# Performance work log

Hardware: AMD Instinct MI355X
Metric: run time of the kernel (lower is better)

The kernel has to match this reference:

```python
import jax, jax.numpy as jnp
import numpy as np

DIM = 768
HID = 3072
HID2 = HID // 2
MAX_LEVEL = 8
N_LEV = MAX_LEVEL + 1
BATCH, SEQ = 2, 2048
EPS = 1e-5


def _layernorm(x, gamma, beta):
    m = jnp.mean(x, axis=-1, keepdims=True)
    v = jnp.mean(jnp.square(x - m), axis=-1, keepdims=True)
    return (x - m) * jax.lax.rsqrt(v + EPS) * gamma + beta


def setup_inputs() -> dict:
    key = jax.random.key(0)
    ks = jax.random.split(key, 12)
    s = 0.02
    return {
        "x": jax.random.normal(ks[0], (BATCH, SEQ, DIM), dtype=jnp.float32),
        "levels_info": jax.random.randint(ks[1], (SEQ, 4), 0, N_LEV, dtype=jnp.int32),
        "gamma": jnp.ones((DIM,), dtype=jnp.float32),
        "beta": jnp.zeros((DIM,), dtype=jnp.float32),
        "W1": jax.random.normal(ks[2], (DIM, HID), dtype=jnp.float32) * s,
        "b1": jnp.zeros((HID,), dtype=jnp.float32),
        "W2": jax.random.normal(ks[3], (HID, DIM), dtype=jnp.float32) * s,
        "b2": jnp.zeros((DIM,), dtype=jnp.float32),
        "A1": jax.random.normal(ks[4], (N_LEV, DIM, HID2), dtype=jnp.float32) * s,
        "a1b": jnp.zeros((N_LEV, HID2), dtype=jnp.float32),
        "A2": jax.random.normal(ks[5], (N_LEV, HID2, DIM), dtype=jnp.float32) * s,
        "a2b": jnp.zeros((N_LEV, DIM), dtype=jnp.float32),
        "lmw": jnp.ones((N_LEV,), dtype=jnp.float32)
        + jax.random.normal(ks[6], (N_LEV,), dtype=jnp.float32) * 0.1,
    }


def reference(x, levels_info, gamma, beta, W1, b1, W2, b2, A1, a1b, A2, a2b, lmw):
    # x: [B,S,D]
    x_norm = _layernorm(x, gamma, beta)
    # main MLP: Linear -> GELU (exact, torch default) -> Linear; dropout=0 is identity
    h = jax.nn.gelu(jnp.einsum("bsd,dh->bsh", x_norm, W1) + b1, approximate=False)
    main_out = jnp.einsum("bsh,hd->bsd", h, W2) + b2

    # per-token depth-indexed adapter routing
    depths = jnp.clip(levels_info[:, 0], 0, MAX_LEVEL)  # [S]
    level_adapted = jnp.zeros_like(main_out)
    for lvl in range(N_LEV):  # small fixed expert set
        mask = (depths == lvl).astype(x.dtype)[None, :, None]  # [1,S,1]
        hl = jax.nn.relu(jnp.einsum("bsd,dh->bsh", x_norm, A1[lvl]) + a1b[lvl])
        level_adapted = level_adapted + mask * (
            jnp.einsum("bsh,hd->bsd", hl, A2[lvl]) + a2b[lvl]
        )

    # softmax over the sequence axis (faithful to F.softmax(..., dim=0))
    mix = jax.nn.softmax(lmw[depths], axis=0)[None, :, None]  # [1,S,1]
    return main_out * (1.0 - mix) + level_adapted * mix
```

## Files before the change

### kernel.cpp

```cpp
#include <hip/hip_runtime.h>
#include <hip/hip_bf16.h>
#include <math.h>

typedef __bf16 bf16;
typedef __bf16 bf16x4 __attribute__((ext_vector_type(4)));
typedef __bf16 bf16x8 __attribute__((ext_vector_type(8)));
typedef float f32x4 __attribute__((ext_vector_type(4)));

#define DIM 768
#define HID 3072
#define HID2 1536
#define NLEV 9
#define SEQ 2048
#define ROWS 4096
#define MAXPAD 5248
#define MAXTILES 41

__device__ __forceinline__ void gld16(const void* g, void* l) {
    __builtin_amdgcn_global_load_lds(
        (const __attribute__((address_space(1))) void*)g,
        (__attribute__((address_space(3))) void*)l, 16, 0, 0);
}

__device__ __forceinline__ float fast_gelu(float v) {
    float v2 = v * v;
    float twou = v * (1.59576912f + 0.071354816f * v2);
    float t = __expf(twou);
    return v * t / (t + 1.0f);
}


__device__ __forceinline__ void ln4_body(int blk,
                                         const float* __restrict__ x,
                                         const float* __restrict__ gamma,
                                         const float* __restrict__ beta,
                                         bf16* __restrict__ xn) {
    int tid = threadIdx.x;
    int wv = tid >> 6, ln = tid & 63;
    int row = blk * 4 + wv;
    const float* xr = x + (size_t)row * DIM;
    int c = ln * 4;
    float4 v0 = *(const float4*)(xr + c);
    float4 v1 = *(const float4*)(xr + c + 256);
    float4 v2 = *(const float4*)(xr + c + 512);
    float s = v0.x + v0.y + v0.z + v0.w
            + v1.x + v1.y + v1.z + v1.w
            + v2.x + v2.y + v2.z + v2.w;
    float q = v0.x * v0.x + v0.y * v0.y + v0.z * v0.z + v0.w * v0.w
            + v1.x * v1.x + v1.y * v1.y + v1.z * v1.z + v1.w * v1.w
            + v2.x * v2.x + v2.y * v2.y + v2.z * v2.z + v2.w * v2.w;
#pragma unroll
    for (int off = 32; off; off >>= 1) {
        s += __shfl_xor(s, off, 64);
        q += __shfl_xor(q, off, 64);
    }
    float m = s * (1.0f / DIM);
    float r = rsqrtf(q * (1.0f / DIM) - m * m + 1e-5f);
    bf16* xo = xn + (size_t)row * DIM;
#pragma unroll
    for (int p = 0; p < 3; p++) {
        int cc = c + p * 256;
        float4 v = (p == 0) ? v0 : (p == 1) ? v1 : v2;
        float4 g = *(const float4*)(gamma + cc);
        float4 b = *(const float4*)(beta + cc);
        bf16x4 o;
        o[0] = (bf16)((v.x - m) * r * g.x + b.x);
        o[1] = (bf16)((v.y - m) * r * g.y + b.y);
        o[2] = (bf16)((v.z - m) * r * g.z + b.z);
        o[3] = (bf16)((v.w - m) * r * g.w + b.w);
        *(bf16x4*)(xo + cc) = o;
    }
}

__device__ __forceinline__ void transpose_body64(bf16* sm,
                                                 const float* __restrict__ inb,
                                                 bf16* __restrict__ outb,
                                                 int R, int C, int bx, int by) {
    int tid = threadIdx.x;
    int ty = tid >> 4;
    int tx4 = (tid & 15) * 4;
#pragma unroll
    for (int p = 0; p < 4; p++) {
        int rloc = p * 16 + ty;
        int row = by * 64 + rloc;
        float4 v = *(const float4*)(inb + (size_t)row * C + bx * 64 + tx4);
        bf16x4 o;
        o[0] = (bf16)v.x; o[1] = (bf16)v.y; o[2] = (bf16)v.z; o[3] = (bf16)v.w;
        *(bf16x4*)(sm + rloc * 68 + tx4) = o;
    }
    __syncthreads();
    int ch = tid & 7;
    int ocb = tid >> 3;
#pragma unroll
    for (int p = 0; p < 2; p++) {
        int oc = p * 32 + ocb;
        bf16x8 tmp;
#pragma unroll
        for (int k = 0; k < 8; k++) tmp[k] = sm[(ch * 8 + k) * 68 + oc];
        *(bf16x8*)(outb + (size_t)(bx * 64 + oc) * R + by * 64 + ch * 8) = tmp;
    }
}

__device__ __forceinline__ void routing_body(float* sm,
                                             const int* __restrict__ levels_info,
                                             const float* __restrict__ lmw,
                                             float* __restrict__ mix,
                                             int* __restrict__ row_index,
                                             int* __restrict__ tile_meta,
                                             float* __restrict__ zbuf) {
    int* cnt = (int*)sm;
    int* cur = cnt + NLEV;
    int* off = cur + NLEV;
    float* mixv = (float*)(off + NLEV);
    int tid = threadIdx.x;
    if (tid < NLEV) { cnt[tid] = 0; cur[tid] = 0; }
    __syncthreads();
    for (int s = tid; s < SEQ; s += 256) {
        int d = levels_info[s * 4];
        d = d < 0 ? 0 : (d > 8 ? 8 : d);
        atomicAdd(&cnt[d], 1);
    }
    for (int i = tid; i < MAXPAD; i += 256) row_index[i] = -1;
    for (int i = tid; i < 512; i += 256) zbuf[i] = 0.0f;
    __syncthreads();
    if (tid == 0) {
        float mx = lmw[0];
        for (int l = 1; l < NLEV; l++) mx = fmaxf(mx, lmw[l]);
        float denom = 0.f;
        for (int l = 0; l < NLEV; l++) denom += (float)cnt[l] * expf(lmw[l] - mx);
        float inv = 1.0f / denom;
        int running = 0, t = 0;
        for (int l = 0; l < NLEV; l++) {
            mixv[l] = expf(lmw[l] - mx) * inv;
            off[l] = running;
            int seg = (2 * cnt[l] + 127) & ~127;
            for (int k = 0; k < seg / 128; k++) tile_meta[t++] = l;
            running += seg;
        }
        for (; t < MAXTILES; t++) tile_meta[t] = -1;
    }
    __syncthreads();
    for (int s = tid; s < SEQ; s += 256) {
        int d = levels_info[s * 4];
        d = d < 0 ? 0 : (d > 8 ? 8 : d);
        int p = atomicAdd(&cur[d], 2);
        row_index[off[d] + p]     = s;
        row_index[off[d] + p + 1] = s + SEQ;
        mix[s] = mixv[d];
    }
}

__global__ __launch_bounds__(256) void prep_kernel(const float* __restrict__ x,
                                                   const int* __restrict__ levels_info,
                                                   const float* __restrict__ gamma,
                                                   const float* __restrict__ beta,
                                                   const float* __restrict__ W1,
                                                   const float* __restrict__ A1,
                                                   const float* __restrict__ W2,
                                                   const float* __restrict__ A2,
                                                   const float* __restrict__ lmw,
                                                   bf16* __restrict__ Xn,
                                                   bf16* __restrict__ W1t,
                                                   bf16* __restrict__ A1t,
                                                   bf16* __restrict__ W2t,
                                                   bf16* __restrict__ A2t,
                                                   float* __restrict__ mix,
                                                   int* __restrict__ row_index,
                                                   int* __restrict__ tile_meta,
                                                   float* __restrict__ zbuf) {
    __shared__ __align__(16) bf16 tsm[64 * 68];
    int b = blockIdx.x;
    if (b == 0) { routing_body((float*)tsm, levels_info, lmw, mix, row_index, tile_meta, zbuf); return; }
    b -= 1;
    if (b < 1024) { ln4_body(b, x, gamma, beta, Xn); return; }
    b -= 1024;
    if (b < 576) {
        transpose_body64(tsm, W1, W1t, DIM, HID, b % 48, b / 48);
        return;
    }
    b -= 576;
    if (b < 2592) {
        int bz = b / 288, r = b % 288;
        transpose_body64(tsm, A1 + (size_t)bz * DIM * HID2, A1t + (size_t)bz * DIM * HID2,
                         DIM, HID2, r % 24, r / 24);
        return;
    }
    b -= 2592;
    if (b < 576) {
        transpose_body64(tsm, W2, W2t, HID, DIM, b % 12, b / 12);
        return;
    }
    b -= 576;
    {
        int bz = b / 288, r = b % 288;
        transpose_body64(tsm, A2 + (size_t)bz * HID2 * DIM, A2t + (size_t)bz * HID2 * DIM,
                         HID2, DIM, r % 12, r / 12);
    }
}

template<int KT>
__device__ __forceinline__ void gemm_loop_db(const bf16* ga0, const bf16* ga1,
                                             const bf16* gb0, const bf16* gb1,
                                             bf16* As, bf16* Bs,
                                             f32x4 (&acc)[4][4]) {
    int tid = threadIdx.x;
    int wv = tid >> 6;
    int lane = tid & 63;
    int wm = wv >> 1, wn = wv & 1;
    int swz = (lane >> 1) & 3;
    int achunk = ((lane >> 4) ^ swz) * 8;
    int aoff = ((wm * 64) + (lane & 15)) * 32 + achunk;
    int boff = ((wn * 64) + (lane & 15)) * 32 + achunk;
    gld16(ga0, As + wv * 512);
    gld16(ga1, As + 2048 + wv * 512);
    gld16(gb0, Bs + wv * 512);
    gld16(gb1, Bs + 2048 + wv * 512);
    ga0 += 32; ga1 += 32; gb0 += 32; gb1 += 32;
#pragma unroll
    for (int kt = 0; kt < KT; ++kt) {
        __syncthreads();
        const int cur = (kt & 1) << 12;
        const int nxt = cur ^ 4096;
        if (kt + 1 < KT) {
            gld16(ga0, As + nxt + wv * 512);
            gld16(ga1, As + nxt + 2048 + wv * 512);
            gld16(gb0, Bs + nxt + wv * 512);
            gld16(gb1, Bs + nxt + 2048 + wv * 512);
            ga0 += 32; ga1 += 32; gb0 += 32; gb1 += 32;
        }
        bf16x8 af[4], bfr[4];
#pragma unroll
        for (int i = 0; i < 4; i++) af[i] = *(const bf16x8*)(As + cur + aoff + i * 512);
#pragma unroll
        for (int j = 0; j < 4; j++) bfr[j] = *(const bf16x8*)(Bs + cur + boff + j * 512);
#pragma unroll
        for (int i = 0; i < 4; i++)
#pragma unroll
            for (int j = 0; j < 4; j++)
                acc[i][j] = __builtin_amdgcn_mfma_f32_16x16x32_bf16(af[i], bfr[j], acc[i][j], 0, 0, 0);
    }
}

#define ACC_INIT(acc) \
    _Pragma("unroll") for (int i = 0; i < 4; i++) \
    _Pragma("unroll") for (int j = 0; j < 4; j++) acc[i][j] = (f32x4){0.f, 0.f, 0.f, 0.f};

#define SWZ_CG(tid) (((tid) & 3) ^ (((tid) >> 3) & 3))

__device__ __forceinline__ void store_tile(const bf16* cbuf, int lane,
                                           bf16* gptr, int ldg) {
#pragma unroll
    for (int p = 0; p < 8; p++) {
        int lrow = p * 8 + (lane >> 3);
        int chunk = (lane & 7) * 8;
        bf16x8 v = *(const bf16x8*)(cbuf + lrow * 64 + chunk);
        *(bf16x8*)(gptr + (size_t)lrow * ldg + chunk) = v;
    }
}

__global__ __launch_bounds__(256) void mlp1_kernel(const bf16* __restrict__ Xn,
                                                   const bf16* __restrict__ W1t,
                                                   const float* __restrict__ b1,
                                                   bf16* __restrict__ H,
                                                   const bf16* __restrict__ A1t,
                                                   const float* __restrict__ a1b,
                                                   const int* __restrict__ row_index,
                                                   const int* __restrict__ tile_meta,
                                                   const bf16* __restrict__ zbuf,
                                                   bf16* __restrict__ HL) {
    __shared__ __align__(16) bf16 smem[16384];
    bf16* As = smem;
    bf16* Bs = smem + 8192;
    int bid = blockIdx.x, tid = threadIdx.x;
    int r0 = tid >> 2, cg = SWZ_CG(tid);
    int lane = tid & 63, wv = tid >> 6, wm = wv >> 1, wn = wv & 1;
    bf16* cbuf = smem + wv * 4096;

    if (bid < 768) {
        int nb = bid / 32, mb = bid % 32;
        f32x4 acc[4][4];
        ACC_INIT(acc);
        const bf16* ga0 = Xn + (size_t)(mb * 128 + r0) * DIM + cg * 8;
        const bf16* ga1 = ga0 + (size_t)64 * DIM;
        const bf16* gb0 = W1t + (size_t)(nb * 128 + r0) * DIM + cg * 8;
        const bf16* gb1 = gb0 + (size_t)64 * DIM;
        gemm_loop_db<24>(ga0, ga1, gb0, gb1, As, Bs, acc);
        int cbase = nb * 128 + wn * 64 + (lane & 15);
        __syncthreads();
#pragma unroll
        for (int j = 0; j < 4; j++) {
            float bias = b1[cbase + j * 16];
#pragma unroll
            for (int i = 0; i < 4; i++)
#pragma unroll
                for (int r = 0; r < 4; r++) {
                    int lrow = i * 16 + ((lane >> 4) << 2) + r;
                    int lcol = j * 16 + (lane & 15);
                    cbuf[lrow * 64 + lcol] = (bf16)fast_gelu(acc[i][j][r] + bias);
                }
        }
        __syncthreads();
        store_tile(cbuf, lane, H + (size_t)(mb * 128 + wm * 64) * HID + nb * 128 + wn * 64, HID);
    } else {
        int t2 = bid - 768;
        int nb = t2 % 12, t = t2 / 12;
        int lvl = tile_meta[t];
        if (lvl < 0) return;
        f32x4 acc[4][4];
        ACC_INIT(acc);
        int ridx0 = row_index[t * 128 + r0];
        int ridx1 = row_index[t * 128 + 64 + r0];
        const bf16* ga0 = (ridx0 >= 0) ? (Xn + (size_t)ridx0 * DIM + cg * 8) : (zbuf + cg * 8);
        const bf16* ga1 = (ridx1 >= 0) ? (Xn + (size_t)ridx1 * DIM + cg * 8) : (zbuf + cg * 8);
        const bf16* Bl = A1t + (size_t)lvl * HID2 * DIM;
        const bf16* gb0 = Bl + (size_t)(nb * 128 + r0) * DIM + cg * 8;
        const bf16* gb1 = gb0 + (size_t)64 * DIM;
        gemm_loop_db<24>(ga0, ga1, gb0, gb1, As, Bs, acc);
        int cbase = nb * 128 + wn * 64 + (lane & 15);
        __syncthreads();
#pragma unroll
        for (int j = 0; j < 4; j++) {
            float bias = a1b[lvl * HID2 + cbase + j * 16];
#pragma unroll
            for (int i = 0; i < 4; i++)
#pragma unroll
                for (int r = 0; r < 4; r++) {
                    int lrow = i * 16 + ((lane >> 4) << 2) + r;
                    int lcol = j * 16 + (lane & 15);
                    cbuf[lrow * 64 + lcol] = (bf16)fmaxf(acc[i][j][r] + bias, 0.0f);
                }
        }
        __syncthreads();
        store_tile(cbuf, lane, HL + (size_t)(t * 128 + wm * 64) * HID2 + nb * 128 + wn * 64, HID2);
    }
}

__global__ __launch_bounds__(256) void mlp2_kernel(const bf16* __restrict__ H,
                                                   const bf16* __restrict__ W2t,
                                                   bf16* __restrict__ part,
                                                   const bf16* __restrict__ HL,
                                                   const bf16* __restrict__ A2t,
                                                   const float* __restrict__ a2b,
                                                   const int* __restrict__ row_index,
                                                   const int* __restrict__ tile_meta,
                                                   bf16* __restrict__ apart) {
    __shared__ __align__(16) bf16 smem[16384];
    bf16* As = smem;
    bf16* Bs = smem + 8192;
    int bid = blockIdx.x, tid = threadIdx.x;
    int r0 = tid >> 2, cg = SWZ_CG(tid);
    int lane = tid & 63, wv = tid >> 6, wm = wv >> 1, wn = wv & 1;
    bf16* cbuf = smem + wv * 4096;
    f32x4 acc[4][4];
    ACC_INIT(acc);

    if (bid < 384) {
        int cc = bid % 12;
        int nb = cc >> 1, ks = cc & 1;
        int mb = bid / 12;
        const bf16* ga0 = H + (size_t)(mb * 128 + r0) * HID + ks * 1536 + cg * 8;
        const bf16* ga1 = ga0 + (size_t)64 * HID;
        const bf16* gb0 = W2t + (size_t)(nb * 128 + r0) * HID + ks * 1536 + cg * 8;
        const bf16* gb1 = gb0 + (size_t)64 * HID;
        gemm_loop_db<48>(ga0, ga1, gb0, gb1, As, Bs, acc);
        __syncthreads();
#pragma unroll
        for (int j = 0; j < 4; j++)
#pragma unroll
            for (int i = 0; i < 4; i++)
#pragma unroll
                for (int r = 0; r < 4; r++) {
                    int lrow = i * 16 + ((lane >> 4) << 2) + r;
                    int lcol = j * 16 + (lane & 15);
                    cbuf[lrow * 64 + lcol] = (bf16)acc[i][j][r];
                }
        __syncthreads();
        bf16* pk = part + (size_t)ks * ROWS * DIM;
        store_tile(cbuf, lane, pk + (size_t)(mb * 128 + wm * 64) * DIM + nb * 128 + wn * 64, DIM);
    } else {
        int t2 = bid - 384;
        int nb = t2 % 6, t = t2 / 6;
        int lvl = tile_meta[t];
        if (lvl < 0) return;
        const bf16* ga0 = HL + (size_t)(t * 128 + r0) * HID2 + cg * 8;
        const bf16* ga1 = ga0 + (size_t)64 * HID2;
        const bf16* Bl = A2t + (size_t)lvl * DIM * HID2;
        const bf16* gb0 = Bl + (size_t)(nb * 128 + r0) * HID2 + cg * 8;
        const bf16* gb1 = gb0 + (size_t)64 * HID2;
        gemm_loop_db<48>(ga0, ga1, gb0, gb1, As, Bs, acc);
        int cbase = nb * 128 + wn * 64 + (lane & 15);
        __syncthreads();
#pragma unroll
        for (int j = 0; j < 4; j++) {
            float bias = a2b[lvl * DIM + cbase + j * 16];
#pragma unroll
            for (int i = 0; i < 4; i++)
#pragma unroll
                for (int r = 0; r < 4; r++) {
                    int lrow = i * 16 + ((lane >> 4) << 2) + r;
                    int lcol = j * 16 + (lane & 15);
                    cbuf[lrow * 64 + lcol] = (bf16)(acc[i][j][r] + bias);
                }
        }
        __syncthreads();
        int colg = nb * 128 + wn * 64;
#pragma unroll
        for (int p = 0; p < 8; p++) {
            int lrow = p * 8 + (lane >> 3);
            int chunk = (lane & 7) * 8;
            int rg = row_index[t * 128 + wm * 64 + lrow];
            if (rg >= 0) {
                bf16x8 v = *(const bf16x8*)(cbuf + lrow * 64 + chunk);
                *(bf16x8*)(apart + (size_t)rg * DIM + colg + chunk) = v;
            }
        }
    }
}

__global__ __launch_bounds__(256) void combine_kernel(const bf16* __restrict__ part,
                                                      const bf16* __restrict__ apart,
                                                      const float* __restrict__ b2,
                                                      const float* __restrict__ mix,
                                                      float* __restrict__ out) {
    int i = blockIdx.x * 256 + threadIdx.x;
    int base = i * 4;
    int row = base / DIM;
    int c = base - row * DIM;
    float mx = mix[row & (SEQ - 1)];
    bf16x4 p0 = *(const bf16x4*)(part + base);
    bf16x4 p1 = *(const bf16x4*)(part + (size_t)ROWS * DIM + base);
    bf16x4 a0 = *(const bf16x4*)(apart + base);
    float4 o;
    float* po = &o.x;
#pragma unroll
    for (int k = 0; k < 4; k++) {
        float main_v = (float)p0[k] + (float)p1[k] + b2[c + k];
        po[k] = (1.0f - mx) * main_v + mx * (float)a0[k];
    }
    *(float4*)(out + base) = o;
}

extern "C" void kernel_launch(void* const* d_in, const int* in_sizes, int n_in,
                              void* d_out, int out_size, void* d_ws, size_t ws_size,
                              hipStream_t stream) {
    const float* x    = (const float*)d_in[0];
    const int* levels = (const int*)d_in[1];
    const float* gamma= (const float*)d_in[2];
    const float* beta = (const float*)d_in[3];
    const float* W1   = (const float*)d_in[4];
    const float* b1   = (const float*)d_in[5];
    const float* W2   = (const float*)d_in[6];
    const float* b2   = (const float*)d_in[7];
    const float* A1   = (const float*)d_in[8];
    const float* a1b  = (const float*)d_in[9];
    const float* A2   = (const float*)d_in[10];
    const float* a2b  = (const float*)d_in[11];
    const float* lmw  = (const float*)d_in[12];
    float* out = (float*)d_out;

    char* p = (char*)d_ws;
    auto alloc = [&](size_t bytes) {
        char* r = p;
        p += (bytes + 255) & ~(size_t)255;
        return r;
    };
    bf16* Xn   = (bf16*)alloc((size_t)ROWS * DIM * 2);
    bf16* W1t  = (bf16*)alloc((size_t)HID * DIM * 2);
    bf16* W2t  = (bf16*)alloc((size_t)DIM * HID * 2);
    bf16* A1t  = (bf16*)alloc((size_t)NLEV * HID2 * DIM * 2);
    bf16* A2t  = (bf16*)alloc((size_t)NLEV * DIM * HID2 * 2);
    bf16* H    = (bf16*)alloc((size_t)ROWS * HID * 2);
    bf16* HL   = (bf16*)alloc((size_t)MAXPAD * HID2 * 2);
    bf16* part = (bf16*)alloc((size_t)2 * ROWS * DIM * 2);
    bf16* apart= (bf16*)alloc((size_t)ROWS * DIM * 2);
    float* mix = (float*)alloc(SEQ * 4);
    int* row_index = (int*)alloc(MAXPAD * 4);
    int* tile_meta = (int*)alloc(MAXTILES * 4);
    float* zbuf    = (float*)alloc(2048);

    prep_kernel<<<dim3(1 + 1024 + 576 + 2592 + 576 + 2592), dim3(256), 0, stream>>>(
        x, levels, gamma, beta, W1, A1, W2, A2, lmw,
        Xn, W1t, A1t, W2t, A2t, mix, row_index, tile_meta, zbuf);

    mlp1_kernel<<<dim3(768 + 492), dim3(256), 0, stream>>>(
        Xn, W1t, b1, H, A1t, a1b, row_index, tile_meta, (const bf16*)zbuf, HL);

    mlp2_kernel<<<dim3(384 + MAXTILES * 6), dim3(256), 0, stream>>>(
        H, W2t, part, HL, A2t, a2b, row_index, tile_meta, apart);

    combine_kernel<<<dim3(ROWS * DIM / 1024), dim3(256), 0, stream>>>(
        part, apart, b2, mix, out);
}
```

Before: 280.6 us.

## Deepen GEMM K-tile to 64, add XCD block swizzle and grouped tile ordering

The double-buffered GEMM loop now stages 64-wide K slices instead of 32, which halves the number of barrier-separated iterations and doubles LDS use per block. The LDS layout changes to an XOR swizzle across 8 chunks. Block IDs are remapped with an XCD-aware swizzle, and the main MLP1 tiles are grouped so that neighbouring blocks share A/B panels in L2. The larger LDS footprint may lower occupancy, and the zero buffer is enlarged to cover 64-element reads for padded rows.

```diff
diff --git a/kernel.cpp b/kernel.cpp
--- a/kernel.cpp
+++ b/kernel.cpp
@@ -27,6 +27,12 @@
     float twou = v * (1.59576912f + 0.071354816f * v2);
     float t = __expf(twou);
     return v * t / (t + 1.0f);
+}
+
+__device__ __forceinline__ int xcd_swizzle(int s, int nwg) {
+    int q = nwg >> 3, r = nwg & 7;
+    int x = s & 7, i = s >> 3;
+    return (x < r ? x * (q + 1) : r * (q + 1) + (x - r) * q) + i;
 }
 
 
@@ -121,7 +127,7 @@
         atomicAdd(&cnt[d], 1);
     }
     for (int i = tid; i < MAXPAD; i += 256) row_index[i] = -1;
-    for (int i = tid; i < 512; i += 256) zbuf[i] = 0.0f;
+    for (int i = tid; i < 1024; i += 256) zbuf[i] = 0.0f;
     __syncthreads();
     if (tid == 0) {
         float mx = lmw[0];
@@ -199,53 +205,56 @@
 }
 
 template<int KT>
-__device__ __forceinline__ void gemm_loop_db(const bf16* ga0, const bf16* ga1,
-                                             const bf16* gb0, const bf16* gb1,
-                                             bf16* As, bf16* Bs,
-                                             f32x4 (&acc)[4][4]) {
+__device__ __forceinline__ void gemm_loop_db64(const bf16* (&ga)[4], const bf16* (&gb)[4],
+                                               bf16* As, bf16* Bs,
+                                               f32x4 (&acc)[4][4]) {
     int tid = threadIdx.x;
     int wv = tid >> 6;
     int lane = tid & 63;
     int wm = wv >> 1, wn = wv & 1;
-    int swz = (lane >> 1) & 3;
-    int achunk = ((lane >> 4) ^ swz) * 8;
-    int aoff = ((wm * 64) + (lane & 15)) * 32 + achunk;
-    int boff = ((wn * 64) + (lane & 15)) * 32 + achunk;
-    gld16(ga0, As + wv * 512);
-    gld16(ga1, As + 2048 + wv * 512);
-    gld16(gb0, Bs + wv * 512);
-    gld16(gb1, Bs + 2048 + wv * 512);
-    ga0 += 32; ga1 += 32; gb0 += 32; gb1 += 32;
+    int r = lane & 15;
+    int ch0 = ((lane >> 4) ^ (lane & 7)) * 8;
+    int aoff = (wm * 64 + r) * 64 + ch0;
+    int boff = (wn * 64 + r) * 64 + ch0;
+#pragma unroll
+    for (int c = 0; c < 4; c++) {
+        gld16(ga[c], As + (c * 32 + wv * 8) * 64);
+        gld16(gb[c], Bs + (c * 32 + wv * 8) * 64);
+        ga[c] += 64; gb[c] += 64;
+    }
 #pragma unroll
     for (int kt = 0; kt < KT; ++kt) {
         __syncthreads();
-        const int cur = (kt & 1) << 12;
-        const int nxt = cur ^ 4096;
+        const int cur = (kt & 1) << 13;
+        const int nxt = cur ^ 8192;
         if (kt + 1 < KT) {
-            gld16(ga0, As + nxt + wv * 512);
-            gld16(ga1, As + nxt + 2048 + wv * 512);
-            gld16(gb0, Bs + nxt + wv * 512);
-            gld16(gb1, Bs + nxt + 2048 + wv * 512);
-            ga0 += 32; ga1 += 32; gb0 += 32; gb1 += 32;
-        }
-        bf16x8 af[4], bfr[4];
-#pragma unroll
-        for (int i = 0; i < 4; i++) af[i] = *(const bf16x8*)(As + cur + aoff + i * 512);
-#pragma unroll
-        for (int j = 0; j < 4; j++) bfr[j] = *(const bf16x8*)(Bs + cur + boff + j * 512);
-#pragma unroll
-        for (int i = 0; i < 4; i++)
-#pragma unroll
-            for (int j = 0; j < 4; j++)
-                acc[i][j] = __builtin_amdgcn_mfma_f32_16x16x32_bf16(af[i], bfr[j], acc[i][j], 0, 0, 0);
+#pragma unroll
+            for (int c = 0; c < 4; c++) {
+                gld16(ga[c], As + nxt + (c * 32 + wv * 8) * 64);
+                gld16(gb[c], Bs + nxt + (c * 32 + wv * 8) * 64);
+                ga[c] += 64; gb[c] += 64;
+            }
+        }
+#pragma unroll
+        for (int k32 = 0; k32 < 2; k32++) {
+            const int kx = k32 << 5;
+            bf16x8 af[4], bfr[4];
+#pragma unroll
+            for (int i = 0; i < 4; i++) af[i] = *(const bf16x8*)(As + cur + ((aoff + i * 1024) ^ kx));
+#pragma unroll
+            for (int j = 0; j < 4; j++) bfr[j] = *(const bf16x8*)(Bs + cur + ((boff + j * 1024) ^ kx));
+#pragma unroll
+            for (int i = 0; i < 4; i++)
+#pragma unroll
+                for (int j = 0; j < 4; j++)
+                    acc[i][j] = __builtin_amdgcn_mfma_f32_16x16x32_bf16(af[i], bfr[j], acc[i][j], 0, 0, 0);
+        }
     }
 }
 
 #define ACC_INIT(acc) \
     _Pragma("unroll") for (int i = 0; i < 4; i++) \
     _Pragma("unroll") for (int j = 0; j < 4; j++) acc[i][j] = (f32x4){0.f, 0.f, 0.f, 0.f};
-
-#define SWZ_CG(tid) (((tid) & 3) ^ (((tid) >> 3) & 3))
 
 __device__ __forceinline__ void store_tile(const bf16* cbuf, int lane,
                                            bf16* gptr, int ldg) {
@@ -268,23 +277,30 @@
                                                    const int* __restrict__ tile_meta,
                                                    const bf16* __restrict__ zbuf,
                                                    bf16* __restrict__ HL) {
-    __shared__ __align__(16) bf16 smem[16384];
+    __shared__ __align__(16) bf16 smem[32768];
     bf16* As = smem;
-    bf16* Bs = smem + 8192;
-    int bid = blockIdx.x, tid = threadIdx.x;
-    int r0 = tid >> 2, cg = SWZ_CG(tid);
+    bf16* Bs = smem + 16384;
+    int bid = xcd_swizzle(blockIdx.x, 1260);
+    int tid = threadIdx.x;
     int lane = tid & 63, wv = tid >> 6, wm = wv >> 1, wn = wv & 1;
+    int lrow = lane >> 3;
+    int lch = ((lane & 7) ^ lrow) * 8;
     bf16* cbuf = smem + wv * 4096;
 
     if (bid < 768) {
-        int nb = bid / 32, mb = bid % 32;
+        int s = bid >> 5, u = bid & 31;
+        int nb = (s % 6) * 4 + (u & 3);
+        int mb = (s / 6) * 8 + (u >> 2);
         f32x4 acc[4][4];
         ACC_INIT(acc);
-        const bf16* ga0 = Xn + (size_t)(mb * 128 + r0) * DIM + cg * 8;
-        const bf16* ga1 = ga0 + (size_t)64 * DIM;
-        const bf16* gb0 = W1t + (size_t)(nb * 128 + r0) * DIM + cg * 8;
-        const bf16* gb1 = gb0 + (size_t)64 * DIM;
-        gemm_loop_db<24>(ga0, ga1, gb0, gb1, As, Bs, acc);
+        const bf16* ga[4]; const bf16* gb[4];
+#pragma unroll
+        for (int c = 0; c < 4; c++) {
+            int rt = c * 32 + wv * 8 + lrow;
+            ga[c] = Xn  + (size_t)(mb * 128 + rt) * DIM + lch;
+            gb[c] = W1t + (size_t)(nb * 128 + rt) * DIM + lch;
+        }
+        gemm_loop_db64<12>(ga, gb, As, Bs, acc);
         int cbase = nb * 128 + wn * 64 + (lane & 15);
         __syncthreads();
 #pragma unroll
@@ -294,9 +310,9 @@
             for (int i = 0; i < 4; i++)
 #pragma unroll
                 for (int r = 0; r < 4; r++) {
-                    int lrow = i * 16 + ((lane >> 4) << 2) + r;
-                    int lcol = j * 16 + (lane & 15);
-                    cbuf[lrow * 64 + lcol] = (bf16)fast_gelu(acc[i][j][r] + bias);
+                    int lr = i * 16 + ((lane >> 4) << 2) + r;
+                    int lc = j * 16 + (lane & 15);
+                    cbuf[lr * 64 + lc] = (bf16)fast_gelu(acc[i][j][r] + bias);
                 }
         }
         __syncthreads();
@@ -308,14 +324,16 @@
         if (lvl < 0) return;
         f32x4 acc[4][4];
         ACC_INIT(acc);
-        int ridx0 = row_index[t * 128 + r0];
-        int ridx1 = row_index[t * 128 + 64 + r0];
-        const bf16* ga0 = (ridx0 >= 0) ? (Xn + (size_t)ridx0 * DIM + cg * 8) : (zbuf + cg * 8);
-        const bf16* ga1 = (ridx1 >= 0) ? (Xn + (size_t)ridx1 * DIM + cg * 8) : (zbuf + cg * 8);
+        const bf16* ga[4]; const bf16* gb[4];
         const bf16* Bl = A1t + (size_t)lvl * HID2 * DIM;
-        const bf16* gb0 = Bl + (size_t)(nb * 128 + r0) * DIM + cg * 8;
-        const bf16* gb1 = gb0 + (size_t)64 * DIM;
-        gemm_loop_db<24>(ga0, ga1, gb0, gb1, As, Bs, acc);
+#pragma unroll
+        for (int c = 0; c < 4; c++) {
+            int rt = c * 32 + wv * 8 + lrow;
+            int rg = row_index[t * 128 + rt];
+            ga[c] = (rg >= 0) ? (Xn + (size_t)rg * DIM + lch) : (zbuf + lch);
+            gb[c] = Bl + (size_t)(nb * 128 + rt) * DIM + lch;
+        }
+        gemm_loop_db64<12>(ga, gb, As, Bs, acc);
         int cbase = nb * 128 + wn * 64 + (lane & 15);
         __syncthreads();
 #pragma unroll
@@ -325,9 +343,9 @@
             for (int i = 0; i < 4; i++)
 #pragma unroll
                 for (int r = 0; r < 4; r++) {
-                    int lrow = i * 16 + ((lane >> 4) << 2) + r;
-                    int lcol = j * 16 + (lane & 15);
-                    cbuf[lrow * 64 + lcol] = (bf16)fmaxf(acc[i][j][r] + bias, 0.0f);
+                    int lr = i * 16 + ((lane >> 4) << 2) + r;
+                    int lc = j * 16 + (lane & 15);
+                    cbuf[lr * 64 + lc] = (bf16)fmaxf(acc[i][j][r] + bias, 0.0f);
                 }
         }
         __syncthreads();
@@ -344,12 +362,14 @@
                                                    const int* __restrict__ row_index,
                                                    const int* __restrict__ tile_meta,
                                                    bf16* __restrict__ apart) {
-    __shared__ __align__(16) bf16 smem[16384];
+    __shared__ __align__(16) bf16 smem[32768];
     bf16* As = smem;
-    bf16* Bs = smem + 8192;
-    int bid = blockIdx.x, tid = threadIdx.x;
-    int r0 = tid >> 2, cg = SWZ_CG(tid);
+    bf16* Bs = smem + 16384;
+    int bid = xcd_swizzle(blockIdx.x, 384 + MAXTILES * 6);
+    int tid = threadIdx.x;
     int lane = tid & 63, wv = tid >> 6, wm = wv >> 1, wn = wv & 1;
+    int lrow = lane >> 3;
+    int lch = ((lane & 7) ^ lrow) * 8;
     bf16* cbuf = smem + wv * 4096;
     f32x4 acc[4][4];
     ACC_INIT(acc);
@@ -358,11 +378,14 @@
         int cc = bid % 12;
         int nb = cc >> 1, ks = cc & 1;
         int mb = bid / 12;
-        const bf16* ga0 = H + (size_t)(mb * 128 + r0) * HID + ks * 1536 + cg * 8;
-        const bf16* ga1 = ga0 + (size_t)64 * HID;
-        const bf16* gb0 = W2t + (size_t)(nb * 128 + r0) * HID + ks * 1536 + cg * 8;
-        const bf16* gb1 = gb0 + (size_t)64 * HID;
-        gemm_loop_db<48>(ga0, ga1, gb0, gb1, As, Bs, acc);
+        const bf16* ga[4]; const bf16* gb[4];
+#pragma unroll
+        for (int c = 0; c < 4; c++) {
+            int rt = c * 32 + wv * 8 + lrow;
+            ga[c] = H   + (size_t)(mb * 128 + rt) * HID + ks * 1536 + lch;
+            gb[c] = W2t + (size_t)(nb * 128 + rt) * HID + ks * 1536 + lch;
+        }
+        gemm_loop_db64<24>(ga, gb, As, Bs, acc);
         __syncthreads();
 #pragma unroll
         for (int j = 0; j < 4; j++)
@@ -370,9 +393,9 @@
             for (int i = 0; i < 4; i++)
 #pragma unroll
                 for (int r = 0; r < 4; r++) {
-                    int lrow = i * 16 + ((lane >> 4) << 2) + r;
-                    int lcol = j * 16 + (lane & 15);
-                    cbuf[lrow * 64 + lcol] = (bf16)acc[i][j][r];
+                    int lr = i * 16 + ((lane >> 4) << 2) + r;
+                    int lc = j * 16 + (lane & 15);
+                    cbuf[lr * 64 + lc] = (bf16)acc[i][j][r];
                 }
         __syncthreads();
         bf16* pk = part + (size_t)ks * ROWS * DIM;
@@ -382,12 +405,15 @@
         int nb = t2 % 6, t = t2 / 6;
         int lvl = tile_meta[t];
         if (lvl < 0) return;
-        const bf16* ga0 = HL + (size_t)(t * 128 + r0) * HID2 + cg * 8;
-        const bf16* ga1 = ga0 + (size_t)64 * HID2;
+        const bf16* ga[4]; const bf16* gb[4];
         const bf16* Bl = A2t + (size_t)lvl * DIM * HID2;
-        const bf16* gb0 = Bl + (size_t)(nb * 128 + r0) * HID2 + cg * 8;
-        const bf16* gb1 = gb0 + (size_t)64 * HID2;
-        gemm_loop_db<48>(ga0, ga1, gb0, gb1, As, Bs, acc);
+#pragma unroll
+        for (int c = 0; c < 4; c++) {
+            int rt = c * 32 + wv * 8 + lrow;
+            ga[c] = HL + (size_t)(t * 128 + rt) * HID2 + lch;
+            gb[c] = Bl + (size_t)(nb * 128 + rt) * HID2 + lch;
+        }
+        gemm_loop_db64<24>(ga, gb, As, Bs, acc);
         int cbase = nb * 128 + wn * 64 + (lane & 15);
         __syncthreads();
 #pragma unroll
@@ -397,20 +423,20 @@
             for (int i = 0; i < 4; i++)
 #pragma unroll
                 for (int r = 0; r < 4; r++) {
-                    int lrow = i * 16 + ((lane >> 4) << 2) + r;
-                    int lcol = j * 16 + (lane & 15);
-                    cbuf[lrow * 64 + lcol] = (bf16)(acc[i][j][r] + bias);
+                    int lr = i * 16 + ((lane >> 4) << 2) + r;
+                    int lc = j * 16 + (lane & 15);
+                    cbuf[lr * 64 + lc] = (bf16)(acc[i][j][r] + bias);
                 }
         }
         __syncthreads();
         int colg = nb * 128 + wn * 64;
 #pragma unroll
         for (int p = 0; p < 8; p++) {
-            int lrow = p * 8 + (lane >> 3);
+            int lr = p * 8 + (lane >> 3);
             int chunk = (lane & 7) * 8;
-            int rg = row_index[t * 128 + wm * 64 + lrow];
+            int rg = row_index[t * 128 + wm * 64 + lr];
             if (rg >= 0) {
-                bf16x8 v = *(const bf16x8*)(cbuf + lrow * 64 + chunk);
+                bf16x8 v = *(const bf16x8*)(cbuf + lr * 64 + chunk);
                 *(bf16x8*)(apart + (size_t)rg * DIM + colg + chunk) = v;
             }
         }
@@ -476,7 +502,7 @@
     float* mix = (float*)alloc(SEQ * 4);
     int* row_index = (int*)alloc(MAXPAD * 4);
     int* tile_meta = (int*)alloc(MAXTILES * 4);
-    float* zbuf    = (float*)alloc(2048);
+    float* zbuf    = (float*)alloc(4096);
 
     prep_kernel<<<dim3(1 + 1024 + 576 + 2592 + 576 + 2592), dim3(256), 0, stream>>>(
         x, levels, gamma, beta, W1, A1, W2, A2, lmw,
```

After: 259.2 us, median of 3. -7.6%, faster.
